# Performance work log

Hardware: AMD Instinct MI355X
Metric: run time of the kernel (lower is better)

Reference implementation:

```python
import jax, jax.numpy as jnp
import numpy as np

N_INNER, N_OUTER = 384, 192  # log-spaced samples as in render()
N_RAYS = 1024
EPS = 1e-10

def _z_vals():
    # torch.logspace is base-10, matching jnp.logspace
    return jnp.concatenate([jnp.logspace(-1.2, 0.0, N_INNER),
                            jnp.logspace(0.0, 2.0, N_OUTER)]).astype(jnp.float32)  # [N]

def _z_lin():
    z = jnp.concatenate([jnp.linspace(-1.2, 0.0, N_INNER),
                         jnp.linspace(0.0, 2.0, N_OUTER)]).astype(jnp.float32)
    return (z + 1.2) / 3.2  # normalized to [0,1], [N]

def _render_rays(sigmas, rgbs, z_vals):
    # Standard alpha compositing (reconstruction of helpers.render_rays_log_new)
    deltas = jnp.diff(z_vals)                                   # [N-1]
    deltas = jnp.concatenate([deltas, jnp.full((1,), 1e10, deltas.dtype)])  # [N]
    alpha = 1.0 - jnp.exp(-sigmas * deltas[None, :])            # [R,N]
    # exclusive cumulative transmittance
    trans = jnp.cumprod(1.0 - alpha + EPS, axis=1)
    trans = jnp.concatenate([jnp.ones_like(trans[:, :1]), trans[:, :-1]], axis=1)
    weights = alpha * trans                                     # [R,N]
    image = jnp.einsum('rn,rnc->rc', weights, rgbs)             # [R,3]
    invdepth = jnp.sum(weights / z_vals[None, :], axis=1)       # [R]
    return image, invdepth, weights

def setup_inputs() -> dict:
    key = jax.random.key(0)
    k1, k2 = jax.random.split(key)
    sigmas = jax.random.uniform(k1, (N_RAYS, N_INNER + N_OUTER), dtype=jnp.float32)
    rgbs = jax.random.uniform(k2, (N_RAYS, N_INNER + N_OUTER, 3), dtype=jnp.float32)
    return {"sigmas": sigmas, "rgbs": rgbs}

def reference(sigmas, rgbs):
    z_vals = _z_vals()
    image, invdepth, weights = _render_rays(sigmas, rgbs, z_vals)
    # distortion loss: sum_ij w_i w_j |t_i - t_j| per ray.
    # Original does bmm(w[:,:,None], w[:,None,:]) * |ti-tj| then sum -> O(R*N^2) memory.
    # Identical math via w^T S w: (weights @ S) then row-dot, no [R,N,N] tensor.
    z_lin = _z_lin()
    S = jnp.abs(z_lin[:, None] - z_lin[None, :])                # [N,N]
    l_per_ray = jnp.sum(weights * (weights @ S), axis=1)        # [R]
    l_dist = jnp.mean(l_per_ray)
    return image[None, ...], invdepth[None, ...], l_dist
```

## Files before the change

### kernel.cpp

```cpp
#include <hip/hip_runtime.h>


#define NSAMP 576
#define NRAYS 1024
#define RPB 4

__device__ __forceinline__ float zexp(int i) {
    if (i < 384) return -1.2f + (float)i * (1.2f / 383.0f);
    return (float)(i - 384) * (2.0f / 191.0f);
}

__global__ __launch_bounds__(256) void render_kernel(
    const float* __restrict__ sigmas,
    const float* __restrict__ rgbs,
    float* __restrict__ out,
    float* __restrict__ wsum)
{
    const float L10 = 3.3219280948873623f;
    const float LE  = 1.4426950408889634f;
    __shared__ float lds[RPB * 2304];

    const int lane = threadIdx.x & 63;
    const int wid  = threadIdx.x >> 6;
    const int ray  = blockIdx.x * RPB + wid;
    float* my = lds + wid * 2304;

    const float4* sig4 = (const float4*)(sigmas + (size_t)ray * NSAMP);
    const float4* rgb4 = (const float4*)(rgbs  + (size_t)ray * NSAMP * 3);
    float4* ls = (float4*)my;
    float4* lr = (float4*)(my + NSAMP);

    float4 s0 = sig4[lane];
    float4 s1 = sig4[64 + lane];
    float4 s2; if (lane < 16) s2 = sig4[128 + lane];
    float4 r0 = rgb4[lane],        r1 = rgb4[64 + lane],  r2 = rgb4[128 + lane];
    float4 r3 = rgb4[192 + lane],  r4 = rgb4[256 + lane], r5 = rgb4[320 + lane];
    float4 r6; if (lane < 48) r6 = rgb4[384 + lane];

    ls[lane] = s0; ls[64 + lane] = s1; if (lane < 16) ls[128 + lane] = s2;
    lr[lane] = r0; lr[64 + lane] = r1; lr[128 + lane] = r2;
    lr[192 + lane] = r3; lr[256 + lane] = r4; lr[320 + lane] = r5;
    if (lane < 48) lr[384 + lane] = r6;
    __syncthreads();

    const int sbase = lane * 9;
    float z[10];
    #pragma unroll
    for (int j = 0; j < 10; ++j) z[j] = exp2f(zexp(sbase + j) * L10);

    float om[9], al[9], t[9], rz[9];
    float Pin = 1.0f;
    #pragma unroll
    for (int j = 0; j < 9; ++j) {
        const int s = sbase + j;
        const float e0 = zexp(s);
        t[j]  = (e0 + 1.2f) * (1.0f / 3.2f);
        rz[j] = exp2f(-e0 * L10);
        const float dlt = (s == NSAMP - 1) ? 1e10f : (z[j + 1] - z[j]);
        const float sg = my[s - sbase + sbase];
        const float e = exp2f(-my[s] * dlt * LE);
        (void)sg;
        al[j] = 1.0f - e;
        om[j] = e + 1e-10f;
        Pin *= om[j];
    }

    float inc = Pin;
    #pragma unroll
    for (int off = 1; off < 64; off <<= 1) {
        float o = __shfl_up(inc, off, 64);
        if (lane >= off) inc *= o;
    }
    float Tcar = __shfl_up(inc, 1, 64);
    if (lane == 0) Tcar = 1.0f;

    float w[9];
    float swl = 0.f, imR = 0.f, imG = 0.f, imB = 0.f, invd = 0.f;
    {
        float cur = Tcar;
        #pragma unroll
        for (int j = 0; j < 9; ++j) {
            const int s = sbase + j;
            const float wk = al[j] * cur;
            cur *= om[j];
            w[j] = wk;
            swl += wk;
            imR += wk * my[NSAMP + s * 3 + 0];
            imG += wk * my[NSAMP + s * 3 + 1];
            imB += wk * my[NSAMP + s * 3 + 2];
            invd += wk * rz[j];
        }
    }

    float incs = swl;
    #pragma unroll
    for (int off = 1; off < 64; off <<= 1) {
        float a = __shfl_up(incs, off, 64);
        if (lane >= off) incs += a;
    }
    const float Sw = __shfl(incs, 63, 64);
    float runW = incs - swl;

    float dist = 0.f;
    #pragma unroll
    for (int j = 0; j < 9; ++j) {
        dist += w[j] * t[j] * (2.0f * runW + w[j] - Sw);
        runW += w[j];
    }

    #pragma unroll
    for (int off = 32; off; off >>= 1) {
        imR  += __shfl_down(imR,  off, 64);
        imG  += __shfl_down(imG,  off, 64);
        imB  += __shfl_down(imB,  off, 64);
        invd += __shfl_down(invd, off, 64);
        dist += __shfl_down(dist, off, 64);
    }

    if (lane == 0) {
        out[ray * 3 + 0] = imR;
        out[ray * 3 + 1] = imG;
        out[ray * 3 + 2] = imB;
        out[3 * NRAYS + ray] = invd;
        wsum[ray] = 2.0f * dist;
    }
}

__global__ __launch_bounds__(64) void reduce_kernel(
    const float* __restrict__ wsum, float* __restrict__ out)
{
    const int lane = threadIdx.x;
    const float4* w4 = (const float4*)wsum;
    float4 a = w4[lane], b = w4[64 + lane], c = w4[128 + lane], d = w4[192 + lane];
    float v = (a.x + a.y + a.z + a.w) + (b.x + b.y + b.z + b.w)
            + (c.x + c.y + c.z + c.w) + (d.x + d.y + d.z + d.w);
    #pragma unroll
    for (int off = 32; off; off >>= 1) v += __shfl_down(v, off, 64);
    if (lane == 0) out[3 * NRAYS + NRAYS] = v * (1.0f / 1024.0f);
}

extern "C" void kernel_launch(void* const* d_in, const int* in_sizes, int n_in,
                              void* d_out, int out_size, void* d_ws, size_t ws_size,
                              hipStream_t stream) {
    const float* sigmas = (const float*)d_in[0];
    const float* rgbs   = (const float*)d_in[1];
    float* out = (float*)d_out;
    float* ws  = (float*)d_ws;

    render_kernel<<<NRAYS / RPB, 256, 0, stream>>>(sigmas, rgbs, out, ws);
    reduce_kernel<<<1, 64, 0, stream>>>(ws, out);
}
```

Before: 11.58 us.

## Load samples directly into registers and compute z values by geometric recurrence

Removes the LDS staging buffer and __syncthreads: each lane now reads its own 9 sigmas and 27 rgb values straight from global memory into registers. The per-sample exp2 calls for z, 1/z and the deltas become multiplicative recurrences with precomputed ratios, leaving one exp2 per sample for alpha. Per-lane strided loads (stride 9/27 floats) are less coalesced than the old float4 loads, and the recurrence adds some floating-point drift.

```diff
diff --git a/kernel.cpp b/kernel.cpp
--- a/kernel.cpp
+++ b/kernel.cpp
@@ -4,10 +4,21 @@
 #define NSAMP 576
 #define NRAYS 1024
 #define RPB 4
+#define NBLK (NRAYS / RPB)
+
+#define ST1 (1.2f / 383.0f)
+#define ST2 (2.0f / 191.0f)
+#define RHO1 1.0072404524f
+#define RHO2 1.0244038551f
+#define IR1  0.9928115948f
+#define IR2  0.9761775050f
+#define RM1LE1 0.0104457650f
+#define RM1LE2 0.0352073200f
+#define E10LE  1.4426950409e10f
 
 __device__ __forceinline__ float zexp(int i) {
-    if (i < 384) return -1.2f + (float)i * (1.2f / 383.0f);
-    return (float)(i - 384) * (2.0f / 191.0f);
+    if (i < 384) return -1.2f + (float)i * ST1;
+    return (float)(i - 384) * ST2;
 }
 
 __global__ __launch_bounds__(256) void render_kernel(
@@ -17,52 +28,46 @@
     float* __restrict__ wsum)
 {
     const float L10 = 3.3219280948873623f;
-    const float LE  = 1.4426950408889634f;
-    __shared__ float lds[RPB * 2304];
-
     const int lane = threadIdx.x & 63;
     const int wid  = threadIdx.x >> 6;
     const int ray  = blockIdx.x * RPB + wid;
-    float* my = lds + wid * 2304;
 
-    const float4* sig4 = (const float4*)(sigmas + (size_t)ray * NSAMP);
-    const float4* rgb4 = (const float4*)(rgbs  + (size_t)ray * NSAMP * 3);
-    float4* ls = (float4*)my;
-    float4* lr = (float4*)(my + NSAMP);
+    const float* __restrict__ sig = sigmas + (size_t)ray * NSAMP + lane * 9;
+    const float* __restrict__ rgb = rgbs  + (size_t)ray * NSAMP * 3 + lane * 27;
 
-    float4 s0 = sig4[lane];
-    float4 s1 = sig4[64 + lane];
-    float4 s2; if (lane < 16) s2 = sig4[128 + lane];
-    float4 r0 = rgb4[lane],        r1 = rgb4[64 + lane],  r2 = rgb4[128 + lane];
-    float4 r3 = rgb4[192 + lane],  r4 = rgb4[256 + lane], r5 = rgb4[320 + lane];
-    float4 r6; if (lane < 48) r6 = rgb4[384 + lane];
-
-    ls[lane] = s0; ls[64 + lane] = s1; if (lane < 16) ls[128 + lane] = s2;
-    lr[lane] = r0; lr[64 + lane] = r1; lr[128 + lane] = r2;
-    lr[192 + lane] = r3; lr[256 + lane] = r4; lr[320 + lane] = r5;
-    if (lane < 48) lr[384 + lane] = r6;
-    __syncthreads();
+    float sg[9], cr[9], cg[9], cb[9];
+    #pragma unroll
+    for (int j = 0; j < 9; ++j) sg[j] = sig[j];
+    #pragma unroll
+    for (int j = 0; j < 9; ++j) {
+        cr[j] = rgb[3 * j + 0];
+        cg[j] = rgb[3 * j + 1];
+        cb[j] = rgb[3 * j + 2];
+    }
 
     const int sbase = lane * 9;
-    float z[10];
-    #pragma unroll
-    for (int j = 0; j < 10; ++j) z[j] = exp2f(zexp(sbase + j) * L10);
+    const float e00 = zexp(sbase);
+    float zc  = exp2f(e00 * L10);
+    float rzc = exp2f(-e00 * L10);
+    float tc  = (e00 + 1.2f) * (1.0f / 3.2f);
 
     float om[9], al[9], t[9], rz[9];
     float Pin = 1.0f;
     #pragma unroll
     for (int j = 0; j < 9; ++j) {
         const int s = sbase + j;
-        const float e0 = zexp(s);
-        t[j]  = (e0 + 1.2f) * (1.0f / 3.2f);
-        rz[j] = exp2f(-e0 * L10);
-        const float dlt = (s == NSAMP - 1) ? 1e10f : (z[j + 1] - z[j]);
-        const float sg = my[s - sbase + sbase];
-        const float e = exp2f(-my[s] * dlt * LE);
-        (void)sg;
+        const bool in1 = (s < 383), bd = (s == 383);
+        t[j]  = tc;
+        rz[j] = rzc;
+        const float coef = in1 ? RM1LE1 : (bd ? 0.0f : RM1LE2);
+        const float a = (s == NSAMP - 1) ? E10LE : zc * coef;
+        const float e = exp2f(-sg[j] * a);
         al[j] = 1.0f - e;
         om[j] = e + 1e-10f;
         Pin *= om[j];
+        zc  *= in1 ? RHO1 : (bd ? 1.0f : RHO2);
+        rzc *= in1 ? IR1  : (bd ? 1.0f : IR2);
+        tc  += (in1 ? ST1 : (bd ? 0.0f : ST2)) * (1.0f / 3.2f);
     }
 
     float inc = Pin;
@@ -80,14 +85,13 @@
         float cur = Tcar;
         #pragma unroll
         for (int j = 0; j < 9; ++j) {
-            const int s = sbase + j;
             const float wk = al[j] * cur;
             cur *= om[j];
             w[j] = wk;
             swl += wk;
-            imR += wk * my[NSAMP + s * 3 + 0];
-            imG += wk * my[NSAMP + s * 3 + 1];
-            imB += wk * my[NSAMP + s * 3 + 2];
+            imR += wk * cr[j];
+            imG += wk * cg[j];
+            imB += wk * cb[j];
             invd += wk * rz[j];
         }
     }
@@ -147,6 +151,6 @@
     float* out = (float*)d_out;
     float* ws  = (float*)d_ws;
 
-    render_kernel<<<NRAYS / RPB, 256, 0, stream>>>(sigmas, rgbs, out, ws);
+    render_kernel<<<NBLK, 256, 0, stream>>>(sigmas, rgbs, out, ws);
     reduce_kernel<<<1, 64, 0, stream>>>(ws, out);
 }
```

Result: faster. 11.00 us (-5.0%).
